# Kernel optimization log

Measured on AMD Instinct MI355X. Metric: run time of the kernel, lower is better.

The kernel has to match this reference:

```python
import jax, jax.numpy as jnp
import numpy as np

B, C, H, W, K = 16, 256, 64, 64, 31
PAD = K // 2
EPS = 1e-5


def setup_inputs() -> dict:
    key = jax.random.key(0)
    k1, k2, k3 = jax.random.split(key, 3)
    x = jax.random.normal(k1, (B, C, H, W), dtype=jnp.float32)
    dw_w = jax.random.normal(k2, (C, 1, K, K), dtype=jnp.float32) * 0.02
    pw_w = jax.random.normal(k3, (C, C), dtype=jnp.float32) * 0.05
    gamma = jnp.ones((C,), dtype=jnp.float32)
    beta = jnp.zeros((C,), dtype=jnp.float32)
    return {"x": x, "dw_w": dw_w, "gamma": gamma, "beta": beta, "pw_w": pw_w}


def reference(x, dw_w, gamma, beta, pw_w):
    # depthwise 31x31 conv, padding=15, groups=C
    y = jax.lax.conv_general_dilated(
        x, dw_w,
        window_strides=(1, 1),
        padding=[(PAD, PAD), (PAD, PAD)],
        dimension_numbers=("NCHW", "OIHW", "NCHW"),
        feature_group_count=C,
    )
    # BatchNorm2d in training mode: biased batch stats over (N,H,W)
    mean = jnp.mean(y, axis=(0, 2, 3), keepdims=True)
    var = jnp.var(y, axis=(0, 2, 3), keepdims=True)  # biased, as torch uses for normalization
    g = gamma[None, :, None, None]
    b = beta[None, :, None, None]
    yn = (y - mean) * jax.lax.rsqrt(var + EPS) * g + b
    r = jax.nn.relu(yn)
    # pointwise 1x1 conv == channel-mixing matmul
    out = jnp.einsum("oc,bchw->bohw", pw_w, r)
    return out
```

## Files before the change

kernel.cpp:

```cpp
#include <hip/hip_runtime.h>
#include <hip/hip_bf16.h>

namespace {
constexpr int CB   = 256;
constexpr int HWp  = 4096;
constexpr int NB   = 16;

typedef __bf16    bf16x8 __attribute__((ext_vector_type(8)));
typedef float     f32x4  __attribute__((ext_vector_type(4)));
typedef float     f32x16 __attribute__((ext_vector_type(16)));
typedef _Float16  f16x2  __attribute__((ext_vector_type(2)));
typedef _Float16  f16x8  __attribute__((ext_vector_type(8)));

typedef __attribute__((address_space(1))) void gvoid;
typedef __attribute__((address_space(3))) void svoid;

__device__ __forceinline__ unsigned int pack2(float lo, float hi) {
#if __has_builtin(__builtin_amdgcn_cvt_pkrtz)
    return __builtin_bit_cast(unsigned int, __builtin_amdgcn_cvt_pkrtz(lo, hi));
#else
    f16x2 v; v[0] = (_Float16)lo; v[1] = (_Float16)hi;
    return __builtin_bit_cast(unsigned int, v);
#endif
}

constexpr int TOEP_PER_C = 31 * 4 * 64;
constexpr int HALO_U32   = 94 * 64;
}

__global__ __launch_bounds__(256) void prep_kernel(
    const float* __restrict__ pw, __hip_bfloat16* __restrict__ pwb,
    const float* __restrict__ dw, uint4* __restrict__ toep,
    float* __restrict__ gsum)
{
    const int bid = blockIdx.x;
    const int tid = threadIdx.x;
    if (bid < 64) {
        if (bid == 0) { gsum[tid] = 0.f; gsum[256 + tid] = 0.f; }
        const int idx = bid * 256 + tid;
        const float4 v = reinterpret_cast<const float4*>(pw)[idx];
        union { __hip_bfloat16 h[4]; uint2 u; } pk;
        pk.h[0] = __float2bfloat16(v.x); pk.h[1] = __float2bfloat16(v.y);
        pk.h[2] = __float2bfloat16(v.z); pk.h[3] = __float2bfloat16(v.w);
        reinterpret_cast<uint2*>(pwb)[idx] = pk.u;
        return;
    }
    const int flat = (bid - 64) * 256 + tid;
    const int lane = flat & 63;
    const int kq   = (flat >> 6) & 3;
    const int rc   = flat >> 8;
    const int r    = rc % 31;
    const int c    = rc / 31;
    const int i    = lane & 31;
    const int kbase = kq * 16 + (lane >> 5) * 8;

    const float* __restrict__ wr = dw + (size_t)c * 961 + r * 31;
    union { _Float16 h[8]; uint4 u; } out;
#pragma unroll
    for (int e = 0; e < 8; ++e) {
        const int t = kbase + e - i - 1;
        out.h[e] = (t >= 0 && t <= 30) ? (_Float16)wr[t] : (_Float16)0.f;
    }
    toep[flat] = out.u;
}

__global__ __launch_bounds__(256, 3) void dwconv_kernel(
    const float* __restrict__ x, const uint4* __restrict__ toep,
    _Float16* __restrict__ y16, float* __restrict__ gsum, float* __restrict__ gsumsq)
{
    __shared__ unsigned int xs[2 * HALO_U32];

    const int bid = blockIdx.x;
    const int c   = bid & 255;
    const int bp  = bid >> 8;
    const int tid = threadIdx.x;

    for (int idx = tid; idx < 2 * HALO_U32 / 4; idx += 256)
        reinterpret_cast<uint4*>(xs)[idx] = uint4{0, 0, 0, 0};
    __syncthreads();

    {
        const int row = tid >> 2;
        const int q   = tid & 3;
        const int hr  = row + 15;
        const int swz = (hr & 7) << 2;
        const int p0  = (8  + q * 8) ^ swz;
        const int p1  = (12 + q * 8) ^ swz;
#pragma unroll
        for (int img = 0; img < 2; ++img) {
            const float4* src = reinterpret_cast<const float4*>(
                x + ((size_t)((bp * 2 + img) * CB + c)) * HWp + row * 64 + q * 16);
            float4 v0 = src[0], v1 = src[1], v2 = src[2], v3 = src[3];
            uint4 a, b;
            a.x = pack2(v0.x, v0.y); a.y = pack2(v0.z, v0.w);
            a.z = pack2(v1.x, v1.y); a.w = pack2(v1.z, v1.w);
            b.x = pack2(v2.x, v2.y); b.y = pack2(v2.z, v2.w);
            b.z = pack2(v3.x, v3.y); b.w = pack2(v3.z, v3.w);
            unsigned int* base = xs + img * HALO_U32 + hr * 64;
            *reinterpret_cast<uint4*>(base + p0) = a;
            *reinterpret_cast<uint4*>(base + p1) = b;
        }
    }
    __syncthreads();

    const int lane = tid & 63;
    const int wid  = tid >> 6;
    const int j    = lane & 31;
    const int half = lane >> 5;
    const int rowb = wid * 16 + (j >> 1);
    const int colb = (j & 1) * 16 + half * 4;
    const uint4* __restrict__ tp = toep + (size_t)c * TOEP_PER_C + lane;

    f32x16 acc0 = {}, acc1 = {};
    uint4 afA[4];
#pragma unroll
    for (int kq = 0; kq < 4; ++kq) afA[kq] = tp[kq * 64];

#pragma unroll 1
    for (int r = 0; r < 31; ++r) {
        uint4 afB[4];
        if (r < 30) {
#pragma unroll
            for (int kq = 0; kq < 4; ++kq) afB[kq] = tp[((r + 1) * 4 + kq) * 64];
        }
        const int row = rowb + r;
        const int swz = (row & 7) << 2;
        const unsigned int* __restrict__ xr = xs + row * 64;
        f16x8 b0[4], b1[4];
#pragma unroll
        for (int kq = 0; kq < 4; ++kq) {
            const int p = (colb + kq * 8) ^ swz;
            b0[kq] = *reinterpret_cast<const f16x8*>(xr + p);
            b1[kq] = *reinterpret_cast<const f16x8*>(xr + HALO_U32 + p);
        }
#pragma unroll
        for (int kq = 0; kq < 4; ++kq)
            acc0 = __builtin_amdgcn_mfma_f32_32x32x16_f16(
                __builtin_bit_cast(f16x8, afA[kq]), b0[kq], acc0, 0, 0, 0);
#pragma unroll
        for (int kq = 0; kq < 4; ++kq)
            acc1 = __builtin_amdgcn_mfma_f32_32x32x16_f16(
                __builtin_bit_cast(f16x8, afA[kq]), b1[kq], acc1, 0, 0, 0);
        if (r < 30) {
#pragma unroll
            for (int kq = 0; kq < 4; ++kq) afA[kq] = afB[kq];
        }
    }

    const size_t pb0    = ((size_t)(bp * 2 * CB + c)) * HWp;
    const int pixbase   = (rowb * 64 + (j & 1) * 32 + (c << 7)) & 4095;
    const size_t pl0    = pb0 + pixbase + 4 * half;
#pragma unroll
    for (int g = 0; g < 4; ++g) {
        uint2 u0, u1;
        u0.x = pack2(acc0[4 * g + 0], acc0[4 * g + 1]);
        u0.y = pack2(acc0[4 * g + 2], acc0[4 * g + 3]);
        u1.x = pack2(acc1[4 * g + 0], acc1[4 * g + 1]);
        u1.y = pack2(acc1[4 * g + 2], acc1[4 * g + 3]);
        *reinterpret_cast<uint2*>(y16 + pl0 + 8 * g)            = u0;
        *reinterpret_cast<uint2*>(y16 + pl0 + CB * HWp + 8 * g) = u1;
    }

    float s = 0.f, s2 = 0.f;
#pragma unroll
    for (int t = 0; t < 16; ++t) {
        s += acc0[t] + acc1[t];
        s2 = fmaf(acc0[t], acc0[t], s2);
        s2 = fmaf(acc1[t], acc1[t], s2);
    }
#pragma unroll
    for (int off = 32; off > 0; off >>= 1) {
        s  += __shfl_down(s,  off, 64);
        s2 += __shfl_down(s2, off, 64);
    }
    if (lane == 0) {
        atomicAdd(&gsum[c],   s);
        atomicAdd(&gsumsq[c], s2);
    }
}

__global__ __launch_bounds__(256, 4) void gemm_kernel(
    const __hip_bfloat16* __restrict__ pwb, const _Float16* __restrict__ y16,
    const float* __restrict__ gsum, const float* __restrict__ gsumsq,
    const float* __restrict__ gamma, const float* __restrict__ beta,
    float* __restrict__ out)
{
    __shared__ __hip_bfloat16 ldsA[2][128 * 32];
    __shared__ unsigned short  ldsB[2][128 * 32];
    __shared__ float scsh[512];

    const int tid  = threadIdx.x;
    const int lane = tid & 63;
    const int wid  = tid >> 6;
    const int b    = blockIdx.z;
    const int m0   = blockIdx.y * 128;
    const int p0   = blockIdx.x * 128;
    const int wm   = wid >> 1, wn = wid & 1;

    {
        const float inv = 1.f / 65536.f;
        const float mean = gsum[tid] * inv;
        const float var  = gsumsq[tid] * inv - mean * mean;
        const float sc   = gamma[tid] * rsqrtf(var + 1e-5f);
        scsh[tid]       = sc;
        scsh[256 + tid] = beta[tid] - mean * sc;
    }

    f32x4 acc[4][4];
#pragma unroll
    for (int mi = 0; mi < 4; ++mi)
#pragma unroll
        for (int ni = 0; ni < 4; ++ni) acc[mi][ni] = {0.f, 0.f, 0.f, 0.f};

    const int srow = lane >> 2;
    const int scol = (lane & 3) * 8;
    const int fr   = lane & 15;
    const int fk   = (lane >> 4) * 8;
    const int cb   = tid & 31;
    const int pg   = tid >> 5;

    const int rotpix = (p0 + pg * 16 + (cb << 7)) & 4095;
    const _Float16* __restrict__ yb =
        y16 + ((size_t)b * CB + cb) * HWp + rotpix;

    uint4 ya0 = *reinterpret_cast<const uint4*>(yb);
    uint4 ya1 = *reinterpret_cast<const uint4*>(yb + 8);
#pragma unroll
    for (int q = 0; q < 2; ++q) {
        const int issue = wid * 2 + q;
        const int row   = issue * 16 + srow;
        __builtin_amdgcn_global_load_lds(
            (gvoid*)(pwb + (size_t)(m0 + row) * CB + scol),
            (svoid*)(&ldsA[0][issue * 512]), 16, 0, 0);
    }
    __syncthreads();

    for (int ks = 0; ks < 8; ++ks) {
        const int cur = ks & 1;
        const float scv = scsh[ks * 32 + cb];
        const float shv = scsh[256 + ks * 32 + cb];
        const f16x8 h0 = __builtin_bit_cast(f16x8, ya0);
        const f16x8 h1 = __builtin_bit_cast(f16x8, ya1);
        unsigned short rb[16];
#pragma unroll
        for (int e = 0; e < 8; ++e) {
            const __hip_bfloat16 v0 = __float2bfloat16(fmaxf(fmaf((float)h0[e], scv, shv), 0.f));
            const __hip_bfloat16 v1 = __float2bfloat16(fmaxf(fmaf((float)h1[e], scv, shv), 0.f));
            rb[e]     = __builtin_bit_cast(unsigned short, v0);
            rb[8 + e] = __builtin_bit_cast(unsigned short, v1);
        }
        unsigned short* bw = &ldsB[cur][(pg * 16) * 32 + cb];
#pragma unroll
        for (int e = 0; e < 16; ++e) bw[e * 32] = rb[e];

        if (ks < 7) {
            const _Float16* yn = yb + (size_t)(ks + 1) * 32 * HWp;
            ya0 = *reinterpret_cast<const uint4*>(yn);
            ya1 = *reinterpret_cast<const uint4*>(yn + 8);
            const int k0 = (ks + 1) * 32;
#pragma unroll
            for (int q = 0; q < 2; ++q) {
                const int issue = wid * 2 + q;
                const int row   = issue * 16 + srow;
                __builtin_amdgcn_global_load_lds(
                    (gvoid*)(pwb + (size_t)(m0 + row) * CB + k0 + scol),
                    (svoid*)(&ldsA[cur ^ 1][issue * 512]), 16, 0, 0);
            }
        }
        __syncthreads();

        bf16x8 af[4], bfv[4];
#pragma unroll
        for (int mi = 0; mi < 4; ++mi)
            af[mi] = *reinterpret_cast<const bf16x8*>(
                &ldsA[cur][(wm * 64 + mi * 16 + fr) * 32 + fk]);
#pragma unroll
        for (int ni = 0; ni < 4; ++ni)
            bfv[ni] = *reinterpret_cast<const bf16x8*>(
                &ldsB[cur][(wn * 64 + ni * 16 + fr) * 32 + fk]);

#pragma unroll
        for (int mi = 0; mi < 4; ++mi)
#pragma unroll
            for (int ni = 0; ni < 4; ++ni)
                acc[mi][ni] = __builtin_amdgcn_mfma_f32_16x16x32_bf16(
                    af[mi], bfv[ni], acc[mi][ni], 0, 0, 0);
    }

    const int frow = (lane >> 4) * 4;
#pragma unroll
    for (int mi = 0; mi < 4; ++mi)
#pragma unroll
        for (int ni = 0; ni < 4; ++ni)
#pragma unroll
            for (int v = 0; v < 4; ++v) {
                const int o = m0 + wm * 64 + mi * 16 + frow + v;
                const int p = p0 + wn * 64 + ni * 16 + fr;
                out[((size_t)(b * CB + o)) * HWp + p] = acc[mi][ni][v];
            }
}

extern "C" void kernel_launch(void* const* d_in, const int* in_sizes, int n_in,
                              void* d_out, int out_size, void* d_ws, size_t ws_size,
                              hipStream_t stream) {
    (void)in_sizes; (void)n_in; (void)out_size; (void)ws_size;
    const float* x     = (const float*)d_in[0];
    const float* dw    = (const float*)d_in[1];
    const float* gamma = (const float*)d_in[2];
    const float* beta  = (const float*)d_in[3];
    const float* pw    = (const float*)d_in[4];
    float* out = (float*)d_out;

    char* ws = (char*)d_ws;
    uint4* toep   = (uint4*)d_out;
    _Float16* y16 = (_Float16*)ws;
    float* gsum   = (float*)(ws + (size_t)33554432);
    float* gsumsq = gsum + 256;
    __hip_bfloat16* pwb = (__hip_bfloat16*)(ws + (size_t)33554432 + 4096);

    prep_kernel<<<dim3(8000), 256, 0, stream>>>(pw, pwb, dw, toep, gsum);
    dwconv_kernel<<<dim3(2048), 256, 0, stream>>>(x, toep, y16, gsum, gsumsq);
    gemm_kernel<<<dim3(32, 2, NB), 256, 0, stream>>>(pwb, y16, gsum, gsumsq,
                                                     gamma, beta, out);
}
```

Measured before the change: 208.0 us.

## Pad dwconv halo rows instead of XOR swizzle; load GEMM A fragments directly to registers

The depthwise conv halo tile in LDS now uses a 52-u32 padded row stride instead of a 64-wide XOR-swizzled layout. This shrinks LDS use and simplifies address math, and the occupancy hint is raised from 3 to 4 blocks. The pointwise GEMM drops the LDS staging of the weight matrix and loads A fragments straight from global memory into registers, prefetched one k-step ahead. It also replaces __syncthreads with an explicit waitcnt plus barrier, and adds setprio around the MFMA blocks in both kernels. The trade-offs are possible bank conflicts from the padding, redundant global reads of the weights across waves, and higher register pressure, which is why the GEMM occupancy hint drops to 3.

```diff
diff --git a/kernel.cpp b/kernel.cpp
--- a/kernel.cpp
+++ b/kernel.cpp
@@ -11,9 +11,6 @@
 typedef float     f32x16 __attribute__((ext_vector_type(16)));
 typedef _Float16  f16x2  __attribute__((ext_vector_type(2)));
 typedef _Float16  f16x8  __attribute__((ext_vector_type(8)));
-
-typedef __attribute__((address_space(1))) void gvoid;
-typedef __attribute__((address_space(3))) void svoid;
 
 __device__ __forceinline__ unsigned int pack2(float lo, float hi) {
 #if __has_builtin(__builtin_amdgcn_cvt_pkrtz)
@@ -25,7 +22,8 @@
 }
 
 constexpr int TOEP_PER_C = 31 * 4 * 64;
-constexpr int HALO_U32   = 94 * 64;
+constexpr int HROW_U32   = 52;
+constexpr int HALO_U32   = 94 * HROW_U32;
 }
 
 __global__ __launch_bounds__(256) void prep_kernel(
@@ -64,7 +62,7 @@
     toep[flat] = out.u;
 }
 
-__global__ __launch_bounds__(256, 3) void dwconv_kernel(
+__global__ __launch_bounds__(256, 4) void dwconv_kernel(
     const float* __restrict__ x, const uint4* __restrict__ toep,
     _Float16* __restrict__ y16, float* __restrict__ gsum, float* __restrict__ gsumsq)
 {
@@ -83,9 +81,8 @@
         const int row = tid >> 2;
         const int q   = tid & 3;
         const int hr  = row + 15;
-        const int swz = (hr & 7) << 2;
-        const int p0  = (8  + q * 8) ^ swz;
-        const int p1  = (12 + q * 8) ^ swz;
+        const int p0  = 8  + q * 8;
+        const int p1  = 12 + q * 8;
 #pragma unroll
         for (int img = 0; img < 2; ++img) {
             const float4* src = reinterpret_cast<const float4*>(
@@ -96,7 +93,7 @@
             a.z = pack2(v1.x, v1.y); a.w = pack2(v1.z, v1.w);
             b.x = pack2(v2.x, v2.y); b.y = pack2(v2.z, v2.w);
             b.z = pack2(v3.x, v3.y); b.w = pack2(v3.z, v3.w);
-            unsigned int* base = xs + img * HALO_U32 + hr * 64;
+            unsigned int* base = xs + img * HALO_U32 + hr * HROW_U32;
             *reinterpret_cast<uint4*>(base + p0) = a;
             *reinterpret_cast<uint4*>(base + p1) = b;
         }
@@ -123,16 +120,14 @@
 #pragma unroll
             for (int kq = 0; kq < 4; ++kq) afB[kq] = tp[((r + 1) * 4 + kq) * 64];
         }
-        const int row = rowb + r;
-        const int swz = (row & 7) << 2;
-        const unsigned int* __restrict__ xr = xs + row * 64;
+        const unsigned int* __restrict__ xr = xs + (rowb + r) * HROW_U32 + colb;
         f16x8 b0[4], b1[4];
 #pragma unroll
         for (int kq = 0; kq < 4; ++kq) {
-            const int p = (colb + kq * 8) ^ swz;
-            b0[kq] = *reinterpret_cast<const f16x8*>(xr + p);
-            b1[kq] = *reinterpret_cast<const f16x8*>(xr + HALO_U32 + p);
-        }
+            b0[kq] = *reinterpret_cast<const f16x8*>(xr + kq * 8);
+            b1[kq] = *reinterpret_cast<const f16x8*>(xr + HALO_U32 + kq * 8);
+        }
+        __builtin_amdgcn_s_setprio(1);
 #pragma unroll
         for (int kq = 0; kq < 4; ++kq)
             acc0 = __builtin_amdgcn_mfma_f32_32x32x16_f16(
@@ -141,15 +136,16 @@
         for (int kq = 0; kq < 4; ++kq)
             acc1 = __builtin_amdgcn_mfma_f32_32x32x16_f16(
                 __builtin_bit_cast(f16x8, afA[kq]), b1[kq], acc1, 0, 0, 0);
+        __builtin_amdgcn_s_setprio(0);
         if (r < 30) {
 #pragma unroll
             for (int kq = 0; kq < 4; ++kq) afA[kq] = afB[kq];
         }
     }
 
-    const size_t pb0    = ((size_t)(bp * 2 * CB + c)) * HWp;
-    const int pixbase   = (rowb * 64 + (j & 1) * 32 + (c << 7)) & 4095;
-    const size_t pl0    = pb0 + pixbase + 4 * half;
+    const size_t pb0  = ((size_t)(bp * 2 * CB + c)) * HWp;
+    const int pixbase = (rowb * 64 + (j & 1) * 32 + (c << 7)) & 4095;
+    const size_t pl0  = pb0 + pixbase + 4 * half;
 #pragma unroll
     for (int g = 0; g < 4; ++g) {
         uint2 u0, u1;
@@ -179,14 +175,13 @@
     }
 }
 
-__global__ __launch_bounds__(256, 4) void gemm_kernel(
+__global__ __launch_bounds__(256, 3) void gemm_kernel(
     const __hip_bfloat16* __restrict__ pwb, const _Float16* __restrict__ y16,
     const float* __restrict__ gsum, const float* __restrict__ gsumsq,
     const float* __restrict__ gamma, const float* __restrict__ beta,
     float* __restrict__ out)
 {
-    __shared__ __hip_bfloat16 ldsA[2][128 * 32];
-    __shared__ unsigned short  ldsB[2][128 * 32];
+    __shared__ unsigned short ldsB[2][128 * 32];
     __shared__ float scsh[512];
 
     const int tid  = threadIdx.x;
@@ -212,31 +207,38 @@
 #pragma unroll
         for (int ni = 0; ni < 4; ++ni) acc[mi][ni] = {0.f, 0.f, 0.f, 0.f};
 
-    const int srow = lane >> 2;
-    const int scol = (lane & 3) * 8;
-    const int fr   = lane & 15;
-    const int fk   = (lane >> 4) * 8;
-    const int cb   = tid & 31;
-    const int pg   = tid >> 5;
+    const int fr = lane & 15;
+    const int fk = (lane >> 4) * 8;
+    const int cb = tid & 31;
+    const int pg = tid >> 5;
 
     const int rotpix = (p0 + pg * 16 + (cb << 7)) & 4095;
     const _Float16* __restrict__ yb =
         y16 + ((size_t)b * CB + cb) * HWp + rotpix;
+    const __hip_bfloat16* __restrict__ pa =
+        pwb + (size_t)(m0 + wm * 64 + fr) * CB + fk;
 
     uint4 ya0 = *reinterpret_cast<const uint4*>(yb);
     uint4 ya1 = *reinterpret_cast<const uint4*>(yb + 8);
-#pragma unroll
-    for (int q = 0; q < 2; ++q) {
-        const int issue = wid * 2 + q;
-        const int row   = issue * 16 + srow;
-        __builtin_amdgcn_global_load_lds(
-            (gvoid*)(pwb + (size_t)(m0 + row) * CB + scol),
-            (svoid*)(&ldsA[0][issue * 512]), 16, 0, 0);
-    }
+    bf16x8 afc[4];
+#pragma unroll
+    for (int mi = 0; mi < 4; ++mi)
+        afc[mi] = *reinterpret_cast<const bf16x8*>(pa + mi * 16 * CB);
     __syncthreads();
 
+#pragma unroll 1
     for (int ks = 0; ks < 8; ++ks) {
         const int cur = ks & 1;
+        uint4 yn0{}, yn1{}; bf16x8 afn[4];
+        if (ks < 7) {
+            const _Float16* yn = yb + (size_t)(ks + 1) * 32 * HWp;
+            yn0 = *reinterpret_cast<const uint4*>(yn);
+            yn1 = *reinterpret_cast<const uint4*>(yn + 8);
+#pragma unroll
+            for (int mi = 0; mi < 4; ++mi)
+                afn[mi] = *reinterpret_cast<const bf16x8*>(
+                    pa + mi * 16 * CB + (ks + 1) * 32);
+        }
         const float scv = scsh[ks * 32 + cb];
         const float shv = scsh[256 + ks * 32 + cb];
         const f16x8 h0 = __builtin_bit_cast(f16x8, ya0);
@@ -253,38 +255,30 @@
 #pragma unroll
         for (int e = 0; e < 16; ++e) bw[e * 32] = rb[e];
 
-        if (ks < 7) {
-            const _Float16* yn = yb + (size_t)(ks + 1) * 32 * HWp;
-            ya0 = *reinterpret_cast<const uint4*>(yn);
-            ya1 = *reinterpret_cast<const uint4*>(yn + 8);
-            const int k0 = (ks + 1) * 32;
-#pragma unroll
-            for (int q = 0; q < 2; ++q) {
-                const int issue = wid * 2 + q;
-                const int row   = issue * 16 + srow;
-                __builtin_amdgcn_global_load_lds(
-                    (gvoid*)(pwb + (size_t)(m0 + row) * CB + k0 + scol),
-                    (svoid*)(&ldsA[cur ^ 1][issue * 512]), 16, 0, 0);
-            }
-        }
-        __syncthreads();
-
-        bf16x8 af[4], bfv[4];
-#pragma unroll
-        for (int mi = 0; mi < 4; ++mi)
-            af[mi] = *reinterpret_cast<const bf16x8*>(
-                &ldsA[cur][(wm * 64 + mi * 16 + fr) * 32 + fk]);
+        asm volatile("s_waitcnt lgkmcnt(0)" ::: "memory");
+        __builtin_amdgcn_s_barrier();
+        __builtin_amdgcn_sched_barrier(0);
+
+        bf16x8 bfv[4];
 #pragma unroll
         for (int ni = 0; ni < 4; ++ni)
             bfv[ni] = *reinterpret_cast<const bf16x8*>(
                 &ldsB[cur][(wn * 64 + ni * 16 + fr) * 32 + fk]);
 
+        __builtin_amdgcn_s_setprio(1);
 #pragma unroll
         for (int mi = 0; mi < 4; ++mi)
 #pragma unroll
             for (int ni = 0; ni < 4; ++ni)
                 acc[mi][ni] = __builtin_amdgcn_mfma_f32_16x16x32_bf16(
-                    af[mi], bfv[ni], acc[mi][ni], 0, 0, 0);
+                    afc[mi], bfv[ni], acc[mi][ni], 0, 0, 0);
+        __builtin_amdgcn_s_setprio(0);
+
+        if (ks < 7) {
+            ya0 = yn0; ya1 = yn1;
+#pragma unroll
+            for (int mi = 0; mi < 4; ++mi) afc[mi] = afn[mi];
+        }
     }
 
     const int frow = (lane >> 4) * 4;
```

Measured after the change: 211.9 us. No clear change (+1.9%).
